# Kernel optimization log

Measured on AMD Instinct MI355X. Metric: run time of the kernel, lower is better.

## Reference

```python
import jax, jax.numpy as jnp
import numpy as np

K = 128
T_X = 4
DATA_LENGTH = 512
B_GROUPS = 64
B = B_GROUPS * DATA_LENGTH
INV_SQRT2 = 0.7071067811865476  # 1/sqrt(2), haar reconstruction filter coeff


def setup_inputs() -> dict:
    key = jax.random.key(0)
    ks = jax.random.split(key, 9)
    x = jax.random.normal(ks[0], (B, T_X, K), jnp.float32)
    y = jax.random.normal(ks[1], (B, 1, K), jnp.float32)
    s = 1.0 / np.sqrt(K).astype(np.float32)
    Wq = jax.random.normal(ks[2], (K, K), jnp.float32) * s
    Wk = jax.random.normal(ks[3], (K, K), jnp.float32) * s
    Wv = jax.random.normal(ks[4], (K, K), jnp.float32) * s
    conv_w = jax.random.normal(ks[5], (K, 2 * K), jnp.float32) * (1.0 / np.sqrt(2 * K).astype(np.float32))
    conv_b = jax.random.normal(ks[6], (K,), jnp.float32) * 0.01
    bn_gamma = jnp.ones((K,), jnp.float32)
    bn_beta = jnp.zeros((K,), jnp.float32)
    bn_mean = jax.random.normal(ks[7], (K,), jnp.float32) * 0.1
    bn_var = jax.random.uniform(ks[8], (K,), jnp.float32, 0.5, 1.5)
    return dict(x=x, y=y, Wq=Wq, Wk=Wk, Wv=Wv, conv_w=conv_w, conv_b=conv_b,
                bn_gamma=bn_gamma, bn_beta=bn_beta, bn_mean=bn_mean, bn_var=bn_var,
                data_length=DATA_LENGTH)


def _idwt_haar(L, H):
    # inverse 1D haar transform along last dim: (Bg, C, 1, T) -> (Bg, C, 1, 2T)
    even = (L + H) * INV_SQRT2
    odd = (L - H) * INV_SQRT2
    out = jnp.stack([even, odd], axis=-1)  # (..., T, 2)
    return out.reshape(L.shape[:-1] + (L.shape[-1] * 2,))


def reference(x, y, Wq, Wk, Wv, conv_w, conv_b, bn_gamma, bn_beta, bn_mean, bn_var, data_length):
    b, t_x, k = x.shape  # t_x = 4 bands, heads = 1, t_y = 1
    q = jnp.einsum('btk,ok->bto', y, Wq)                      # (b, 1, k)
    keys = jnp.einsum('bsk,ok->bso', x, Wk) * (1.0 / (k ** 0.5))  # (b, 4, k)
    v = jnp.einsum('bsk,ok->bso', x, Wv)                      # (b, 4, k)
    dot = jnp.einsum('bto,bso->bs', q, keys)                  # (b, 4)
    w = jax.nn.softmax(dot, axis=1)                           # softmax over the 4 bands
    outs = w[:, :, None] * v                                  # (b, 4, k) band-weighted values
    Bg = b // data_length
    # per band: (b, k) -> (Bg, dl, 1, k) -> permute -> (Bg, k, 1, dl)
    o = outs.reshape(Bg, data_length, t_x, k).transpose(2, 0, 3, 1)  # (4, Bg, k, dl)
    o = o[:, :, :, None, :]                                   # (4, Bg, k, 1, dl)
    out_L = _idwt_haar(o[0], o[1])                            # (Bg, k, 1, 2*dl)
    out_H = _idwt_haar(o[2], o[3])
    out = jnp.concatenate([out_L, out_H], axis=1)             # (Bg, 2k, 1, 2*dl)
    # transition: 1x1 conv + BN (eval mode) + LeakyReLU(0.01)
    z = jnp.einsum('bcij,oc->boij', out, conv_w) + conv_b[None, :, None, None]
    scale = (bn_gamma * jax.lax.rsqrt(bn_var + 1e-5))[None, :, None, None]
    z = (z - bn_mean[None, :, None, None]) * scale + bn_beta[None, :, None, None]
    return jnp.where(z > 0, z, 0.01 * z)
```

## Files before the change

### kernel.cpp

```cpp
#include <hip/hip_runtime.h>
#include <stdint.h>

typedef __attribute__((ext_vector_type(8))) short bf16x8;
typedef __attribute__((ext_vector_type(4))) float f32x4;

__device__ __forceinline__ unsigned short f2bf(float x) {
    union { float f; uint32_t u; } v; v.f = x;
    uint32_t r = v.u + 0x7FFFu + ((v.u >> 16) & 1u);
    return (unsigned short)(r >> 16);
}
__device__ __forceinline__ uint32_t pack2bf(float a, float b) {
    return (uint32_t)f2bf(a) | ((uint32_t)f2bf(b) << 16);
}
__device__ __forceinline__ float bf2f(uint32_t lo) {
    union { uint32_t u; float f; } v; v.u = lo << 16; return v.f;
}
__device__ __forceinline__ float lrelu(float v) { return v > 0.f ? v : 0.01f * v; }

__global__ __launch_bounds__(256) void precompute_kernel(
    const float* __restrict__ Wq, const float* __restrict__ Wk,
    const float* __restrict__ Wv, const float* __restrict__ conv_w,
    const float* __restrict__ conv_b, const float* __restrict__ bn_gamma,
    const float* __restrict__ bn_beta, const float* __restrict__ bn_mean,
    const float* __restrict__ bn_var,
    unsigned short* __restrict__ Gh, unsigned short* __restrict__ Gl,
    unsigned short* __restrict__ Mh,
    float* __restrict__ scale2, float* __restrict__ bias2)
{
    __shared__ float lds0[2176];
    __shared__ float lds1[2176];
    const int tid = threadIdx.x;
    const int bid = blockIdx.x;

    if (bid == 192) {
        if (tid < 128) {
            float sc = bn_gamma[tid] * rsqrtf(bn_var[tid] + 1e-5f);
            scale2[tid] = sc;
            bias2[tid]  = (conv_b[tid] - bn_mean[tid]) * sc + bn_beta[tid];
        }
        return;
    }

    if (bid < 64) {
        int i0 = (bid >> 3) << 4, j0 = (bid & 7) << 4;
        #pragma unroll
        for (int t = 0; t < 8; ++t) {
            int e = tid + t * 256;
            int o = e >> 4, c = e & 15;
            lds0[o * 17 + c] = Wk[o * 128 + i0 + c];
            lds1[o * 17 + c] = Wq[o * 128 + j0 + c];
        }
        __syncthreads();
        int ti = tid >> 4, tj = tid & 15;
        float sum = 0.f;
        #pragma unroll 8
        for (int o = 0; o < 128; ++o) sum += lds0[o * 17 + ti] * lds1[o * 17 + tj];
        float val = sum * 0.08838834764831845f;
        unsigned short h = f2bf(val);
        int idx = (i0 + ti) * 128 + j0 + tj;
        Gh[idx] = h;
        Gl[idx] = f2bf(val - bf2f(h));
    } else {
        int rel = bid - 64;
        int o0 = (rel >> 4) << 4, c0 = (rel & 15) << 4;
        int cw0 = (c0 >> 7) << 7, cc0 = c0 & 127;
        #pragma unroll
        for (int t = 0; t < 8; ++t) {
            int e = tid + t * 256;
            int to = e >> 7, k = e & 127;
            lds0[to * 132 + k] = conv_w[(o0 + to) * 256 + cw0 + k];
            int kk = e >> 4, c = e & 15;
            lds1[kk * 17 + c] = Wv[kk * 128 + cc0 + c];
        }
        __syncthreads();
        int to = tid >> 4, tc = tid & 15;
        float sum = 0.f;
        #pragma unroll 8
        for (int k = 0; k < 128; ++k) sum += lds0[to * 132 + k] * lds1[k * 17 + tc];
        Mh[(o0 + to) * 256 + c0 + tc] = f2bf(sum * 0.7071067811865476f);
    }
}

#define AADDR(row, gi)   (((row) << 8) + ((((gi) ^ ((row) & 7))) << 4))

__global__ __launch_bounds__(256)
__attribute__((amdgpu_waves_per_eu(4, 4)))
void fused_kernel(
    const float* __restrict__ x, const float* __restrict__ y,
    const unsigned short* __restrict__ Gh, const unsigned short* __restrict__ Gl,
    const unsigned short* __restrict__ Mh,
    const float* __restrict__ scale2, const float* __restrict__ bias2,
    float* __restrict__ out)
{
    __shared__ __align__(16) unsigned char smem[16384];
    float* gbufF = (float*)(smem + 8192);

    const int tid = threadIdx.x;
    const int w = tid >> 6;
    const int l = tid & 63;
    const int quad = l >> 4;
    const int i16 = l & 15;
    const int bid = blockIdx.x;
    const int b0 = bid * 16;
    const int b_loc = 4 * w + quad;

    union F8 { float4 v[2]; float f[8]; };
    F8 X[4];
    {
        const float* xb = x + (size_t)(b0 + b_loc) * 512 + i16 * 8;
        #pragma unroll
        for (int t = 0; t < 4; ++t) {
            X[t].v[0] = *(const float4*)(xb + t * 128);
            X[t].v[1] = *(const float4*)(xb + t * 128 + 4);
        }
    }
    const int ks0 = bid & 3;
    bf16x8 pgh[2], pgl[2];
    #pragma unroll
    for (int n = 0; n < 2; ++n) {
        int off = ((2 * w + n) * 16 + i16) * 128 + ks0 * 32 + quad * 8;
        pgh[n] = *(const bf16x8*)(Gh + off);
        pgl[n] = *(const bf16x8*)(Gl + off);
    }

    {
        int row = tid >> 4, gk = tid & 15;
        const float* yb = y + (size_t)(b0 + row) * 128 + gk * 8;
        float4 v0 = *(const float4*)(yb);
        float4 v1 = *(const float4*)(yb + 4);
        float f[8] = {v0.x, v0.y, v0.z, v0.w, v1.x, v1.y, v1.z, v1.w};
        uint32_t hi[4], lo[4];
        #pragma unroll
        for (int e = 0; e < 4; ++e) {
            unsigned short h0 = f2bf(f[2 * e]), h1 = f2bf(f[2 * e + 1]);
            hi[e] = (uint32_t)h0 | ((uint32_t)h1 << 16);
            lo[e] = (uint32_t)f2bf(f[2 * e] - bf2f(h0)) |
                    ((uint32_t)f2bf(f[2 * e + 1] - bf2f(h1)) << 16);
        }
        int addr = AADDR(row, gk);
        *(uint4*)(smem + addr)        = make_uint4(hi[0], hi[1], hi[2], hi[3]);
        *(uint4*)(smem + 4096 + addr) = make_uint4(lo[0], lo[1], lo[2], lo[3]);
    }
    __syncthreads();

    {
        f32x4 accg[2];
        accg[0] = (f32x4){0.f, 0.f, 0.f, 0.f};
        accg[1] = (f32x4){0.f, 0.f, 0.f, 0.f};
        #pragma unroll
        for (int ks = 0; ks < 4; ++ks) {
            int ksr = (ks + bid) & 3;
            int aaddr = AADDR(i16, ksr * 4 + quad);
            bf16x8 ah = *(const bf16x8*)(smem + aaddr);
            bf16x8 al = *(const bf16x8*)(smem + 4096 + aaddr);
            #pragma unroll
            for (int n = 0; n < 2; ++n) {
                bf16x8 bh, bl;
                if (ks == 0) { bh = pgh[n]; bl = pgl[n]; }
                else {
                    int off = ((2 * w + n) * 16 + i16) * 128 + ksr * 32 + quad * 8;
                    bh = *(const bf16x8*)(Gh + off);
                    bl = *(const bf16x8*)(Gl + off);
                }
                accg[n] = __builtin_amdgcn_mfma_f32_16x16x32_bf16(ah, bh, accg[n], 0, 0, 0);
                accg[n] = __builtin_amdgcn_mfma_f32_16x16x32_bf16(al, bh, accg[n], 0, 0, 0);
                accg[n] = __builtin_amdgcn_mfma_f32_16x16x32_bf16(ah, bl, accg[n], 0, 0, 0);
            }
        }
        #pragma unroll
        for (int n = 0; n < 2; ++n) {
            int i = (2 * w + n) * 16 + i16;
            #pragma unroll
            for (int r = 0; r < 4; ++r)
                gbufF[(quad * 4 + r) * 128 + i] = accg[n][r];
        }
    }
    __syncthreads();

    {
        float4 ga = *(const float4*)(gbufF + b_loc * 128 + i16 * 8);
        float4 gb = *(const float4*)(gbufF + b_loc * 128 + i16 * 8 + 4);
        float p[4];
        #pragma unroll
        for (int t = 0; t < 4; ++t) {
            float4 a = X[t].v[0], b = X[t].v[1];
            p[t] = a.x * ga.x + a.y * ga.y + a.z * ga.z + a.w * ga.w
                 + b.x * gb.x + b.y * gb.y + b.z * gb.z + b.w * gb.w;
        }
        #pragma unroll
        for (int off = 8; off >= 1; off >>= 1) {
            p[0] += __shfl_xor(p[0], off);
            p[1] += __shfl_xor(p[1], off);
            p[2] += __shfl_xor(p[2], off);
            p[3] += __shfl_xor(p[3], off);
        }
        float mx = fmaxf(fmaxf(p[0], p[1]), fmaxf(p[2], p[3]));
        float e0 = __expf(p[0] - mx), e1 = __expf(p[1] - mx);
        float e2 = __expf(p[2] - mx), e3 = __expf(p[3] - mx);
        float inv = 1.f / (e0 + e1 + e2 + e3);
        float w0 = e0 * inv, w1 = e1 * inv, w2 = e2 * inv, w3 = e3 * inv;
        int r0 = 2 * b_loc;
        int a0 = AADDR(r0, i16), a1 = AADDR(r0 + 1, i16);
        uint32_t eL[4], oL[4], eH[4], oH[4];
        #pragma unroll
        for (int e = 0; e < 4; ++e) {
            int c0 = 2 * e, c1 = 2 * e + 1;
            eL[e] = pack2bf(w0 * X[0].f[c0] + w1 * X[1].f[c0], w0 * X[0].f[c1] + w1 * X[1].f[c1]);
            oL[e] = pack2bf(w0 * X[0].f[c0] - w1 * X[1].f[c0], w0 * X[0].f[c1] - w1 * X[1].f[c1]);
            eH[e] = pack2bf(w2 * X[2].f[c0] + w3 * X[3].f[c0], w2 * X[2].f[c1] + w3 * X[3].f[c1]);
            oH[e] = pack2bf(w2 * X[2].f[c0] - w3 * X[3].f[c0], w2 * X[2].f[c1] - w3 * X[3].f[c1]);
        }
        *(uint4*)(smem + a0)        = make_uint4(eL[0], eL[1], eL[2], eL[3]);
        *(uint4*)(smem + a1)        = make_uint4(oL[0], oL[1], oL[2], oL[3]);
        *(uint4*)(smem + 8192 + a0) = make_uint4(eH[0], eH[1], eH[2], eH[3]);
        *(uint4*)(smem + 8192 + a1) = make_uint4(oH[0], oH[1], oH[2], oH[3]);
    }

    const int ks0b = bid & 7;
    bf16x8 pmh[2];
    {
        int half = ks0b >> 2, kk = ks0b & 3;
        #pragma unroll
        for (int n = 0; n < 2; ++n)
            pmh[n] = *(const bf16x8*)(Mh + ((2 * w + n) * 16 + i16) * 256 + half * 128 + kk * 32 + quad * 8);
    }
    __syncthreads();

    f32x4 acc[2][2];
    #pragma unroll
    for (int rb = 0; rb < 2; ++rb)
        #pragma unroll
        for (int n = 0; n < 2; ++n) acc[rb][n] = (f32x4){0.f, 0.f, 0.f, 0.f};

    #pragma unroll
    for (int ks = 0; ks < 8; ++ks) {
        int ksr = (ks + bid) & 7;
        int half = ksr >> 2, kk = ksr & 3;
        int base = half << 13;
        int gi = kk * 4 + quad;
        bf16x8 a0v = *(const bf16x8*)(smem + base + AADDR(i16, gi));
        bf16x8 a1v = *(const bf16x8*)(smem + base + AADDR(16 + i16, gi));
        #pragma unroll
        for (int n = 0; n < 2; ++n) {
            bf16x8 bh;
            if (ks == 0) bh = pmh[n];
            else bh = *(const bf16x8*)(Mh + ((2 * w + n) * 16 + i16) * 256 + half * 128 + kk * 32 + quad * 8);
            acc[0][n] = __builtin_amdgcn_mfma_f32_16x16x32_bf16(a0v, bh, acc[0][n], 0, 0, 0);
            acc[1][n] = __builtin_amdgcn_mfma_f32_16x16x32_bf16(a1v, bh, acc[1][n], 0, 0, 0);
        }
    }

    {
        float* outp = out + (size_t)(bid >> 5) * 131072 + (bid & 31) * 32;
        #pragma unroll
        for (int n = 0; n < 2; ++n) {
            int o = (2 * w + n) * 16 + i16;
            float sc = scale2[o], bi = bias2[o];
            #pragma unroll
            for (int rb = 0; rb < 2; ++rb) {
                int jb = 16 * rb + quad * 4;
                f32x4 a = acc[rb][n];
                float4 r;
                r.x = lrelu(a[0] * sc + bi);
                r.y = lrelu(a[1] * sc + bi);
                r.z = lrelu(a[2] * sc + bi);
                r.w = lrelu(a[3] * sc + bi);
                *(float4*)(outp + (size_t)o * 1024 + jb) = r;
            }
        }
    }
}

extern "C" void kernel_launch(void* const* d_in, const int* in_sizes, int n_in,
                              void* d_out, int out_size, void* d_ws, size_t ws_size,
                              hipStream_t stream)
{
    (void)in_sizes; (void)n_in; (void)out_size; (void)ws_size;
    const float* x        = (const float*)d_in[0];
    const float* y        = (const float*)d_in[1];
    const float* Wq       = (const float*)d_in[2];
    const float* Wk       = (const float*)d_in[3];
    const float* Wv       = (const float*)d_in[4];
    const float* conv_w   = (const float*)d_in[5];
    const float* conv_b   = (const float*)d_in[6];
    const float* bn_gamma = (const float*)d_in[7];
    const float* bn_beta  = (const float*)d_in[8];
    const float* bn_mean  = (const float*)d_in[9];
    const float* bn_var   = (const float*)d_in[10];

    unsigned char* ws = (unsigned char*)d_ws;
    unsigned short* Gh = (unsigned short*)(ws);
    unsigned short* Gl = (unsigned short*)(ws + 32768);
    unsigned short* Mh = (unsigned short*)(ws + 65536);
    float* scale2      = (float*)(ws + 131072);
    float* bias2       = (float*)(ws + 131584);

    hipLaunchKernelGGL(precompute_kernel, dim3(193), dim3(256), 0, stream,
                       Wq, Wk, Wv, conv_w, conv_b, bn_gamma, bn_beta, bn_mean,
                       bn_var, Gh, Gl, Mh, scale2, bias2);
    hipLaunchKernelGGL(fused_kernel, dim3(2048), dim3(256), 0, stream,
                       x, y, Gh, Gl, Mh, scale2, bias2, (float*)d_out);
}
```

Baseline: 158.2 us.

## Stage x through LDS with async global-to-LDS loads and preload G fragments

```diff
diff --git a/kernel.cpp b/kernel.cpp
--- a/kernel.cpp
+++ b/kernel.cpp
@@ -9,13 +9,21 @@
     uint32_t r = v.u + 0x7FFFu + ((v.u >> 16) & 1u);
     return (unsigned short)(r >> 16);
 }
-__device__ __forceinline__ uint32_t pack2bf(float a, float b) {
-    return (uint32_t)f2bf(a) | ((uint32_t)f2bf(b) << 16);
+__device__ __forceinline__ uint32_t cvtpk(float a, float b) {
+    uint32_t r;
+    asm("v_cvt_pk_bf16_f32 %0, %1, %2" : "=v"(r) : "v"(a), "v"(b));
+    return r;
 }
 __device__ __forceinline__ float bf2f(uint32_t lo) {
     union { uint32_t u; float f; } v; v.u = lo << 16; return v.f;
 }
 __device__ __forceinline__ float lrelu(float v) { return v > 0.f ? v : 0.01f * v; }
+
+__device__ __forceinline__ void gload_lds16(const void* g, void* l) {
+    __builtin_amdgcn_global_load_lds(
+        (const __attribute__((address_space(1))) uint32_t*)g,
+        (__attribute__((address_space(3))) uint32_t*)l, 16, 0, 0);
+}
 
 __global__ __launch_bounds__(256) void precompute_kernel(
     const float* __restrict__ Wq, const float* __restrict__ Wk,
@@ -84,7 +92,7 @@
 #define AADDR(row, gi)   (((row) << 8) + ((((gi) ^ ((row) & 7))) << 4))
 
 __global__ __launch_bounds__(256)
-__attribute__((amdgpu_waves_per_eu(4, 4)))
+__attribute__((amdgpu_waves_per_eu(3)))
 void fused_kernel(
     const float* __restrict__ x, const float* __restrict__ y,
     const unsigned short* __restrict__ Gh, const unsigned short* __restrict__ Gl,
@@ -92,8 +100,8 @@
     const float* __restrict__ scale2, const float* __restrict__ bias2,
     float* __restrict__ out)
 {
-    __shared__ __align__(16) unsigned char smem[16384];
-    float* gbufF = (float*)(smem + 8192);
+    __shared__ __align__(16) unsigned char smem[49152];
+    float* gbufF = (float*)(smem + 40960);
 
     const int tid = threadIdx.x;
     const int w = tid >> 6;
@@ -104,31 +112,25 @@
     const int b0 = bid * 16;
     const int b_loc = 4 * w + quad;
 
-    union F8 { float4 v[2]; float f[8]; };
-    F8 X[4];
-    {
-        const float* xb = x + (size_t)(b0 + b_loc) * 512 + i16 * 8;
-        #pragma unroll
-        for (int t = 0; t < 4; ++t) {
-            X[t].v[0] = *(const float4*)(xb + t * 128);
-            X[t].v[1] = *(const float4*)(xb + t * 128 + 4);
-        }
-    }
-    const int ks0 = bid & 3;
-    bf16x8 pgh[2], pgl[2];
+    const int row = tid >> 4, gk = tid & 15;
+    const float* yb = y + (size_t)(b0 + row) * 128 + gk * 8;
+    float4 yv0 = *(const float4*)(yb);
+    float4 yv1 = *(const float4*)(yb + 4);
+
+    bf16x8 pgh[4][2], pgl[4][2];
     #pragma unroll
-    for (int n = 0; n < 2; ++n) {
-        int off = ((2 * w + n) * 16 + i16) * 128 + ks0 * 32 + quad * 8;
-        pgh[n] = *(const bf16x8*)(Gh + off);
-        pgl[n] = *(const bf16x8*)(Gl + off);
-    }
-
-    {
-        int row = tid >> 4, gk = tid & 15;
-        const float* yb = y + (size_t)(b0 + row) * 128 + gk * 8;
-        float4 v0 = *(const float4*)(yb);
-        float4 v1 = *(const float4*)(yb + 4);
-        float f[8] = {v0.x, v0.y, v0.z, v0.w, v1.x, v1.y, v1.z, v1.w};
+    for (int ks = 0; ks < 4; ++ks) {
+        int ksr = (ks + bid) & 3;
+        #pragma unroll
+        for (int n = 0; n < 2; ++n) {
+            int off = ((2 * w + n) * 16 + i16) * 128 + ksr * 32 + quad * 8;
+            pgh[ks][n] = *(const bf16x8*)(Gh + off);
+            pgl[ks][n] = *(const bf16x8*)(Gl + off);
+        }
+    }
+
+    {
+        float f[8] = {yv0.x, yv0.y, yv0.z, yv0.w, yv1.x, yv1.y, yv1.z, yv1.w};
         uint32_t hi[4], lo[4];
         #pragma unroll
         for (int e = 0; e < 4; ++e) {
@@ -138,10 +140,20 @@
                     ((uint32_t)f2bf(f[2 * e + 1] - bf2f(h1)) << 16);
         }
         int addr = AADDR(row, gk);
-        *(uint4*)(smem + addr)        = make_uint4(hi[0], hi[1], hi[2], hi[3]);
-        *(uint4*)(smem + 4096 + addr) = make_uint4(lo[0], lo[1], lo[2], lo[3]);
+        *(uint4*)(smem + 32768 + addr) = make_uint4(hi[0], hi[1], hi[2], hi[3]);
+        *(uint4*)(smem + 36864 + addr) = make_uint4(lo[0], lo[1], lo[2], lo[3]);
     }
     __syncthreads();
+
+    #pragma unroll
+    for (int k = 0; k < 8; ++k) {
+        int c  = w * 8 + k;
+        int s  = c >> 1, hf = c & 1;
+        int p  = hf * 64 + l;
+        int u  = p ^ ((p >> 2) & 6) ^ ((s & 3) << 1);
+        const float* src = x + (size_t)(b0 + s) * 512 + u * 4;
+        gload_lds16(src, smem + s * 2048 + hf * 1024);
+    }
 
     {
         f32x4 accg[2];
@@ -151,20 +163,13 @@
         for (int ks = 0; ks < 4; ++ks) {
             int ksr = (ks + bid) & 3;
             int aaddr = AADDR(i16, ksr * 4 + quad);
-            bf16x8 ah = *(const bf16x8*)(smem + aaddr);
-            bf16x8 al = *(const bf16x8*)(smem + 4096 + aaddr);
+            bf16x8 ah = *(const bf16x8*)(smem + 32768 + aaddr);
+            bf16x8 al = *(const bf16x8*)(smem + 36864 + aaddr);
             #pragma unroll
             for (int n = 0; n < 2; ++n) {
-                bf16x8 bh, bl;
-                if (ks == 0) { bh = pgh[n]; bl = pgl[n]; }
-                else {
-                    int off = ((2 * w + n) * 16 + i16) * 128 + ksr * 32 + quad * 8;
-                    bh = *(const bf16x8*)(Gh + off);
-                    bl = *(const bf16x8*)(Gl + off);
-                }
-                accg[n] = __builtin_amdgcn_mfma_f32_16x16x32_bf16(ah, bh, accg[n], 0, 0, 0);
-                accg[n] = __builtin_amdgcn_mfma_f32_16x16x32_bf16(al, bh, accg[n], 0, 0, 0);
-                accg[n] = __builtin_amdgcn_mfma_f32_16x16x32_bf16(ah, bl, accg[n], 0, 0, 0);
+                accg[n] = __builtin_amdgcn_mfma_f32_16x16x32_bf16(ah, pgh[ks][n], accg[n], 0, 0, 0);
+                accg[n] = __builtin_amdgcn_mfma_f32_16x16x32_bf16(al, pgh[ks][n], accg[n], 0, 0, 0);
+                accg[n] = __builtin_amdgcn_mfma_f32_16x16x32_bf16(ah, pgl[ks][n], accg[n], 0, 0, 0);
             }
         }
         #pragma unroll
@@ -180,10 +185,17 @@
     {
         float4 ga = *(const float4*)(gbufF + b_loc * 128 + i16 * 8);
         float4 gb = *(const float4*)(gbufF + b_loc * 128 + i16 * 8 + 4);
+        float xf[4][8];
         float p[4];
         #pragma unroll
         for (int t = 0; t < 4; ++t) {
-            float4 a = X[t].v[0], b = X[t].v[1];
+            int g0 = t * 32 + i16 * 2;
+            int q  = g0 ^ ((g0 >> 2) & 6) ^ ((b_loc & 3) << 1);
+            const float* xp = (const float*)(smem + b_loc * 2048 + q * 16);
+            float4 a = *(const float4*)xp;
+            float4 b = *(const float4*)(xp + 4);
+            xf[t][0] = a.x; xf[t][1] = a.y; xf[t][2] = a.z; xf[t][3] = a.w;
+            xf[t][4] = b.x; xf[t][5] = b.y; xf[t][6] = b.z; xf[t][7] = b.w;
             p[t] = a.x * ga.x + a.y * ga.y + a.z * ga.z + a.w * ga.w
                  + b.x * gb.x + b.y * gb.y + b.z * gb.z + b.w * gb.w;
         }
@@ -205,15 +217,15 @@
         #pragma unroll
         for (int e = 0; e < 4; ++e) {
             int c0 = 2 * e, c1 = 2 * e + 1;
-            eL[e] = pack2bf(w0 * X[0].f[c0] + w1 * X[1].f[c0], w0 * X[0].f[c1] + w1 * X[1].f[c1]);
-            oL[e] = pack2bf(w0 * X[0].f[c0] - w1 * X[1].f[c0], w0 * X[0].f[c1] - w1 * X[1].f[c1]);
-            eH[e] = pack2bf(w2 * X[2].f[c0] + w3 * X[3].f[c0], w2 * X[2].f[c1] + w3 * X[3].f[c1]);
-            oH[e] = pack2bf(w2 * X[2].f[c0] - w3 * X[3].f[c0], w2 * X[2].f[c1] - w3 * X[3].f[c1]);
-        }
-        *(uint4*)(smem + a0)        = make_uint4(eL[0], eL[1], eL[2], eL[3]);
-        *(uint4*)(smem + a1)        = make_uint4(oL[0], oL[1], oL[2], oL[3]);
-        *(uint4*)(smem + 8192 + a0) = make_uint4(eH[0], eH[1], eH[2], eH[3]);
-        *(uint4*)(smem + 8192 + a1) = make_uint4(oH[0], oH[1], oH[2], oH[3]);
+            eL[e] = cvtpk(w0 * xf[0][c0] + w1 * xf[1][c0], w0 * xf[0][c1] + w1 * xf[1][c1]);
+            oL[e] = cvtpk(w0 * xf[0][c0] - w1 * xf[1][c0], w0 * xf[0][c1] - w1 * xf[1][c1]);
+            eH[e] = cvtpk(w2 * xf[2][c0] + w3 * xf[3][c0], w2 * xf[2][c1] + w3 * xf[3][c1]);
+            oH[e] = cvtpk(w2 * xf[2][c0] - w3 * xf[3][c0], w2 * xf[2][c1] - w3 * xf[3][c1]);
+        }
+        *(uint4*)(smem + 32768 + a0) = make_uint4(eL[0], eL[1], eL[2], eL[3]);
+        *(uint4*)(smem + 32768 + a1) = make_uint4(oL[0], oL[1], oL[2], oL[3]);
+        *(uint4*)(smem + 40960 + a0) = make_uint4(eH[0], eH[1], eH[2], eH[3]);
+        *(uint4*)(smem + 40960 + a1) = make_uint4(oH[0], oH[1], oH[2], oH[3]);
     }
 
     const int ks0b = bid & 7;
@@ -236,7 +248,7 @@
     for (int ks = 0; ks < 8; ++ks) {
         int ksr = (ks + bid) & 7;
         int half = ksr >> 2, kk = ksr & 3;
-        int base = half << 13;
+        int base = 32768 + (half << 13);
         int gi = kk * 4 + quad;
         bf16x8 a0v = *(const bf16x8*)(smem + base + AADDR(i16, gi));
         bf16x8 a1v = *(const bf16x8*)(smem + base + AADDR(16 + i16, gi));
```

After: 158.6 us. About the same (+0.2%).
